# Kernel tuning notes

Hardware: AMD Instinct MI355X
Metric: run time of the kernel (lower is better)

## Reference

```python
import jax, jax.numpy as jnp
import numpy as np

N, D = 32768, 256  # n_nodes, in_dim == mem_dim


def setup_inputs() -> dict:
    key = jax.random.key(0)
    ks = jax.random.split(key, 8)
    inputs = jax.random.normal(ks[0], (N, D), jnp.float32)
    state = jax.random.normal(ks[1], (1, D), jnp.float32)  # initial root cell state
    s = 1.0 / np.sqrt(D)  # pytorch default uniform init bound
    root_W = jax.random.uniform(ks[2], (D, D), jnp.float32, -s, s)
    root_b = jax.random.uniform(ks[3], (D,), jnp.float32, -s, s)
    W_ih = jax.random.uniform(ks[4], (4 * D, D), jnp.float32, -s, s)
    W_hh = jax.random.uniform(ks[5], (4 * D, D), jnp.float32, -s, s)
    b_ih = jax.random.uniform(ks[6], (4 * D,), jnp.float32, -s, s)
    b_hh = jax.random.uniform(ks[7], (4 * D,), jnp.float32, -s, s)
    # topologically ordered random tree: parents[i] < i, node 0 is root
    rng = np.random.default_rng(0)
    raw = rng.integers(0, N, size=N)
    parents = jnp.asarray(np.minimum(raw, np.maximum(np.arange(N) - 1, 0)).astype(np.int64))
    idx = jnp.arange(N, dtype=jnp.int64)  # node -> input row (tree.idx)
    return dict(inputs=inputs, state=state, root_W=root_W, root_b=root_b,
                W_ih=W_ih, W_hh=W_hh, b_ih=b_ih, b_hh=b_hh,
                parents=parents, idx=idx)


def reference(inputs, state, root_W, root_b, W_ih, W_hh, b_ih, b_hh, parents, idx):
    n, d = inputs.shape
    # root: tanh(Linear(inputs[root_idx])), cell state = given state
    h0 = jnp.tanh(inputs[idx[0]] @ root_W.T + root_b)
    c0 = state[0]
    H = jnp.zeros((n, d), inputs.dtype).at[0].set(h0)
    C = jnp.zeros((n, d), inputs.dtype).at[0].set(c0)

    def step(carry, i):
        H, C = carry
        p = parents[i]
        x = inputs[idx[i]]
        # torch nn.LSTMCell: gates = x W_ih^T + b_ih + h W_hh^T + b_hh
        gates = x @ W_ih.T + b_ih + H[p] @ W_hh.T + b_hh
        ig, fg, gg, og = jnp.split(gates, 4)
        c = jax.nn.sigmoid(fg) * C[p] + jax.nn.sigmoid(ig) * jnp.tanh(gg)
        h = jax.nn.sigmoid(og) * jnp.tanh(c)
        return (H.at[i].set(h), C.at[i].set(c)), None

    (H, C), _ = jax.lax.scan(step, (H, C), jnp.arange(1, n))
    # topdown_hidden_traversal: scatter each node's hidden into a [n_inputs, mem_dim] buffer
    hiddens = jnp.zeros((n, d), inputs.dtype).at[idx].set(H)
    # (root topdown_state, root topdown hidden, all hiddens)
    return C[0:1], H[0:1], hiddens
```

## Files before the change

### kernel.cpp

```cpp
#include <hip/hip_runtime.h>


#define NN 32768
#define DD 256
#define GP 1024
#define DSTR 16

typedef __attribute__((ext_vector_type(8))) short short8;
typedef __attribute__((ext_vector_type(4))) float float4_;

static __device__ __forceinline__ unsigned short f2bf(float f) {
    unsigned u = __builtin_bit_cast(unsigned, f);
    unsigned r = u + 0x7FFFu + ((u >> 16) & 1u);
    return (unsigned short)(r >> 16);
}
static __device__ __forceinline__ float bf2f(unsigned short u) {
    unsigned v = ((unsigned)u) << 16;
    return __builtin_bit_cast(float, v);
}
static __device__ __forceinline__ float sigf(float x) { return 1.0f / (1.0f + __expf(-x)); }
static __device__ __forceinline__ float tanh_(float x) { return 1.0f - 2.0f / (__expf(2.0f * x) + 1.0f); }

__global__ void k_init(int* cnt, int* cur, int* done, int* maxd) {
    int g = blockIdx.x * 256 + threadIdx.x;
    if (g < NN + 2) { cnt[g] = 0; cur[g] = 0; }
    if (g < (NN + 2) * DSTR) done[g] = 0;
    if (g == 0) maxd[0] = 0;
}

__global__ void k_root(const float* __restrict__ X, const float* __restrict__ state,
                       const float* __restrict__ rootW, const float* __restrict__ rootb,
                       const int* __restrict__ idx,
                       unsigned short* __restrict__ Hb, float* __restrict__ C, int* __restrict__ done) {
    const int t = threadIdx.x;
    const int row = idx[0];
    const float4_* xr = (const float4_*)(X + (size_t)row * DD);
    const float4_* wr = (const float4_*)(rootW + (size_t)t * DD);
    float acc = rootb[t];
    for (int k = 0; k < DD / 4; ++k) {
        float4_ a = xr[k], b = wr[k];
        acc += a[0] * b[0] + a[1] * b[1] + a[2] * b[2] + a[3] * b[3];
    }
    Hb[t] = f2bf(tanh_(acc));
    C[t] = state[t];
    __syncthreads();
    __threadfence();
    if (t == 0) __hip_atomic_store(&done[0], 8, __ATOMIC_RELEASE, __HIP_MEMORY_SCOPE_AGENT);
}

__global__ void k_dep_init(const int* __restrict__ parents, int* dep, int* jmp) {
    int i = blockIdx.x * 256 + threadIdx.x;
    if (i >= NN) return;
    dep[i] = (i == 0) ? 0 : 1;
    jmp[i] = (i == 0) ? 0 : parents[i];
}

__global__ void k_dep_step(const int* __restrict__ depA, const int* __restrict__ jmpA,
                           int* __restrict__ depB, int* __restrict__ jmpB) {
    int i = blockIdx.x * 256 + threadIdx.x;
    if (i >= NN) return;
    int j = jmpA[i];
    depB[i] = depA[i] + depA[j];
    jmpB[i] = jmpA[j];
}

__global__ void k_hist(const int* __restrict__ dep, int* cnt, int* maxd) {
    int i = blockIdx.x * 256 + threadIdx.x;
    if (i >= NN) return;
    int d = dep[i];
    atomicAdd(&cnt[d], 1);
    atomicMax(&maxd[0], d);
}

__global__ void k_scan(const int* __restrict__ cnt, int* __restrict__ off) {
    __shared__ int sums[256];
    const int tid = threadIdx.x;
    const int base = tid * 128;
    int s = 0;
    for (int k = 0; k < 128; ++k) s += cnt[base + k];
    sums[tid] = s;
    __syncthreads();
    if (tid == 0) {
        int run = 0;
        for (int t = 0; t < 256; ++t) { int tmp = sums[t]; sums[t] = run; run += tmp; }
    }
    __syncthreads();
    int run = sums[tid];
    for (int k = 0; k < 128; ++k) { off[base + k] = run; run += cnt[base + k]; }
    if (tid == 255) off[NN] = run;
}

__global__ void k_scatter(const int* __restrict__ dep, const int* __restrict__ off,
                          int* cur, int* __restrict__ lev) {
    int i = blockIdx.x * 256 + threadIdx.x;
    if (i >= NN) return;
    int d = dep[i];
    int pos = off[d] + atomicAdd(&cur[d], 1);
    lev[pos] = i;
}

__global__ __launch_bounds__(256, 1) void k_gx(
    const float* __restrict__ X, const float* __restrict__ Wih,
    const float* __restrict__ bih, const float* __restrict__ bhh,
    const int* __restrict__ idx, unsigned short* __restrict__ Gp) {
    __shared__ __align__(16) short bw_s[128 * 264];
    __shared__ float bias_s[128];
    const int tid = threadIdx.x;
    const int w = tid >> 6, l = tid & 63;
    const int lanelo = l & 15, quad = l >> 4;

    short8 a[2][8];
    #pragma unroll
    for (int ti = 0; ti < 2; ++ti) {
        int n = (blockIdx.x * 8 + w * 2 + ti) * 16 + lanelo;
        int row = idx[n];
        const float* xp = X + (size_t)row * DD + quad * 8;
        #pragma unroll
        for (int ks = 0; ks < 8; ++ks) {
            float4_ x0 = *(const float4_*)(xp + ks * 32);
            float4_ x1 = *(const float4_*)(xp + ks * 32 + 4);
            short8 s;
            s[0] = f2bf(x0[0]); s[1] = f2bf(x0[1]); s[2] = f2bf(x0[2]); s[3] = f2bf(x0[3]);
            s[4] = f2bf(x1[0]); s[5] = f2bf(x1[1]); s[6] = f2bf(x1[2]); s[7] = f2bf(x1[3]);
            a[ti][ks] = s;
        }
    }
    for (int gc = 0; gc < 8; ++gc) {
        __syncthreads();
        for (int e = tid; e < 128 * 64; e += 256) {
            int r = e >> 6, c4 = (e & 63) * 4;
            float4_ b = *(const float4_*)(Wih + (size_t)(gc * 128 + r) * DD + c4);
            unsigned short* pb = (unsigned short*)&bw_s[r * 264 + c4];
            pb[0] = f2bf(b[0]); pb[1] = f2bf(b[1]); pb[2] = f2bf(b[2]); pb[3] = f2bf(b[3]);
        }
        if (tid < 128) bias_s[tid] = bih[gc * 128 + tid] + bhh[gc * 128 + tid];
        __syncthreads();
        #pragma unroll
        for (int ntl = 0; ntl < 8; ++ntl) {
            float4_ acc0 = (float4_){0.f, 0.f, 0.f, 0.f};
            float4_ acc1 = (float4_){0.f, 0.f, 0.f, 0.f};
            #pragma unroll
            for (int ks = 0; ks < 8; ++ks) {
                short8 bf = *(const short8*)&bw_s[(ntl * 16 + lanelo) * 264 + ks * 32 + quad * 8];
                acc0 = __builtin_amdgcn_mfma_f32_16x16x32_bf16(a[0][ks], bf, acc0, 0, 0, 0);
                acc1 = __builtin_amdgcn_mfma_f32_16x16x32_bf16(a[1][ks], bf, acc1, 0, 0, 0);
            }
            float bia = bias_s[ntl * 16 + lanelo];
            int g = gc * 128 + ntl * 16 + lanelo;
            int nb0 = (blockIdx.x * 8 + w * 2) * 16 + quad * 4;
            #pragma unroll
            for (int r = 0; r < 4; ++r) {
                Gp[(size_t)(nb0 + r) * GP + g] = f2bf(acc0[r] + bia);
                Gp[(size_t)(nb0 + 16 + r) * GP + g] = f2bf(acc1[r] + bia);
            }
        }
    }
}

__global__ __launch_bounds__(256, 1) void k_tree2(
    const float* __restrict__ Whh,
    const int* __restrict__ parents,
    const int* __restrict__ off, const int* __restrict__ lev, const int* __restrict__ maxd_g,
    const unsigned short* __restrict__ Gp,
    unsigned short* __restrict__ Hb, float* __restrict__ C, int* __restrict__ done) {

    __shared__ __align__(16) short w_s[128 * 264];
    __shared__ __align__(16) short A_s[16 * 264];
    __shared__ __align__(16) float G_s[16 * 128];
    __shared__ __align__(16) float R_s[16 * 132];
    __shared__ int nd_s[16], par_s[16];

    const int tid = threadIdx.x;
    const int j = blockIdx.x & 7, grp = blockIdx.x >> 3;
    const int w = tid >> 6, l = tid & 63;
    const int lanelo = l & 15, quad = l >> 4;

    for (int e = tid; e < 128 * 64; e += 256) {
        int r = e >> 6, c4 = (e & 63) * 4;
        int G = ((r >> 5) * 256) + j * 32 + (r & 31);
        float4_ b = *(const float4_*)(Whh + (size_t)G * DD + c4);
        unsigned short* pb = (unsigned short*)&w_s[r * 264 + c4];
        pb[0] = f2bf(b[0]); pb[1] = f2bf(b[1]); pb[2] = f2bf(b[2]); pb[3] = f2bf(b[3]);
    }
    __syncthreads();

    const int maxd = maxd_g[0];
    int prev_lo = off[0], lo = off[1];
    for (int d = 1; d <= maxd; ++d) {
        const int hi = off[d + 1];
        const int tiles = (hi - lo + 15) >> 4;
        if (grp < tiles) {
            const int target = ((lo - prev_lo + 15) >> 4) << 3;
            int ndone = 0;
            for (int t = grp; t < tiles; t += 32) {
                const int base = lo + t * 16;
                if (tid < 16) {
                    int node = -1, p = 0;
                    if (base + tid < hi) { node = lev[base + tid]; p = parents[node]; }
                    nd_s[tid] = node; par_s[tid] = p;
                }
                __syncthreads();
                {
                    int m = tid >> 4, q8 = (tid & 15) * 8;
                    int seg = q8 >> 5, cc = q8 & 31;
                    float4_ g01 = (float4_){0.f, 0.f, 0.f, 0.f};
                    float4_ g23 = (float4_){0.f, 0.f, 0.f, 0.f};
                    if (nd_s[m] >= 0) {
                        const unsigned short* gp =
                            Gp + (size_t)nd_s[m] * GP + seg * 256 + j * 32 + cc;
                        short8 gv = *(const short8*)gp;
                        g01[0] = bf2f(gv[0]); g01[1] = bf2f(gv[1]); g01[2] = bf2f(gv[2]); g01[3] = bf2f(gv[3]);
                        g23[0] = bf2f(gv[4]); g23[1] = bf2f(gv[5]); g23[2] = bf2f(gv[6]); g23[3] = bf2f(gv[7]);
                    }
                    *(float4_*)&G_s[m * 128 + q8] = g01;
                    *(float4_*)&G_s[m * 128 + q8 + 4] = g23;
                }
                if (t == grp) {
                    if (tid == 0) {
                        while (__hip_atomic_load(&done[(d - 1) * DSTR], __ATOMIC_RELAXED,
                                                 __HIP_MEMORY_SCOPE_AGENT) < target)
                            __builtin_amdgcn_s_sleep(1);
                    }
                    __syncthreads();
                    __builtin_amdgcn_fence(__ATOMIC_ACQUIRE, "workgroup");
                }
                float cp0, cp1;
                {
                    int m0 = tid >> 5, c0 = tid & 31, col = j * 32 + c0;
                    cp0 = __hip_atomic_load(&C[(size_t)par_s[m0] * DD + col],
                                            __ATOMIC_RELAXED, __HIP_MEMORY_SCOPE_AGENT);
                    cp1 = __hip_atomic_load(&C[(size_t)par_s[m0 + 8] * DD + col],
                                            __ATOMIC_RELAXED, __HIP_MEMORY_SCOPE_AGENT);
                }
                {
                    const unsigned* HbU = (const unsigned*)Hb;
                    unsigned hv[8];
                    #pragma unroll
                    for (int k2 = 0; k2 < 8; ++k2) {
                        int e = tid + k2 * 256, m = e >> 7, cu = e & 127;
                        hv[k2] = (nd_s[m] >= 0)
                            ? __hip_atomic_load(&HbU[(size_t)par_s[m] * 128 + cu],
                                                __ATOMIC_RELAXED, __HIP_MEMORY_SCOPE_AGENT)
                            : 0u;
                    }
                    #pragma unroll
                    for (int k2 = 0; k2 < 8; ++k2) {
                        int e = tid + k2 * 256, m = e >> 7, cu = e & 127;
                        *(unsigned*)&A_s[m * 264 + cu * 2] = hv[k2];
                    }
                }
                __syncthreads();
                {
                    short8 af[8];
                    #pragma unroll
                    for (int ks = 0; ks < 8; ++ks)
                        af[ks] = *(const short8*)&A_s[lanelo * 264 + ks * 32 + quad * 8];
                    #pragma unroll
                    for (int ti = 0; ti < 2; ++ti) {
                        int ntl = w * 2 + ti;
                        float4_ acc = (float4_){0.f, 0.f, 0.f, 0.f};
                        #pragma unroll
                        for (int ks = 0; ks < 8; ++ks) {
                            short8 bf = *(const short8*)&w_s[(ntl * 16 + lanelo) * 264 + ks * 32 + quad * 8];
                            acc = __builtin_amdgcn_mfma_f32_16x16x32_bf16(af[ks], bf, acc, 0, 0, 0);
                        }
                        #pragma unroll
                        for (int r = 0; r < 4; ++r)
                            R_s[(quad * 4 + r) * 132 + ntl * 16 + lanelo] = acc[r];
                    }
                }
                __syncthreads();
                {
                    int m0 = tid >> 5, c = tid & 31, col = j * 32 + c;
                    #pragma unroll
                    for (int pass = 0; pass < 2; ++pass) {
                        int m = m0 + pass * 8;
                        float cp = pass ? cp1 : cp0;
                        float ig = R_s[m * 132 + c]      + G_s[m * 128 + c];
                        float fg = R_s[m * 132 + 32 + c] + G_s[m * 128 + 32 + c];
                        float gg = R_s[m * 132 + 64 + c] + G_s[m * 128 + 64 + c];
                        float og = R_s[m * 132 + 96 + c] + G_s[m * 128 + 96 + c];
                        float cn = sigf(fg) * cp + sigf(ig) * tanh_(gg);
                        float hn = sigf(og) * tanh_(cn);
                        int node = nd_s[m];
                        unsigned short hs = f2bf(hn);
                        unsigned pair = ((unsigned)hs) |
                                        (((unsigned)(unsigned short)__shfl_down((int)hs, 1)) << 16);
                        if (node >= 0) {
                            __hip_atomic_store(&C[(size_t)node * DD + col], cn,
                                               __ATOMIC_RELAXED, __HIP_MEMORY_SCOPE_AGENT);
                            if ((c & 1) == 0)
                                __hip_atomic_store(&((unsigned*)Hb)[(size_t)node * 128 + (col >> 1)],
                                                   pair, __ATOMIC_RELAXED, __HIP_MEMORY_SCOPE_AGENT);
                        }
                    }
                }
                ndone++;
                __syncthreads();
            }
            __builtin_amdgcn_fence(__ATOMIC_RELEASE, "workgroup");
            if (tid == 0)
                __hip_atomic_fetch_add(&done[d * DSTR], ndone,
                                       __ATOMIC_RELAXED, __HIP_MEMORY_SCOPE_AGENT);
        }
        prev_lo = lo; lo = hi;
    }
}

__global__ void k_out(const unsigned short* __restrict__ Hb, const float* __restrict__ C,
                      const int* __restrict__ idx, float* __restrict__ out) {
    const int b = blockIdx.x, t = threadIdx.x;
    if (b < NN) {
        int drow = idx[b];
        out[512 + (size_t)drow * DD + t] = bf2f(Hb[(size_t)b * DD + t]);
    } else {
        out[t] = C[t];
        out[DD + t] = bf2f(Hb[t]);
    }
}

extern "C" void kernel_launch(void* const* d_in, const int* in_sizes, int n_in,
                              void* d_out, int out_size, void* d_ws, size_t ws_size,
                              hipStream_t stream) {
    const float* X     = (const float*)d_in[0];
    const float* state = (const float*)d_in[1];
    const float* rootW = (const float*)d_in[2];
    const float* rootb = (const float*)d_in[3];
    const float* Wih   = (const float*)d_in[4];
    const float* Whh   = (const float*)d_in[5];
    const float* bih   = (const float*)d_in[6];
    const float* bhh   = (const float*)d_in[7];
    const int* parents = (const int*)d_in[8];
    const int* idx     = (const int*)d_in[9];

    float* C           = (float*)d_ws;
    unsigned short* Hb = (unsigned short*)(C + (size_t)NN * DD);
    unsigned short* Gp = Hb + (size_t)NN * DD;
    int* ip            = (int*)(Gp + (size_t)NN * GP);
    int* depA = ip;            ip += NN;
    int* jmpA = ip;            ip += NN;
    int* depB = ip;            ip += NN;
    int* jmpB = ip;            ip += NN;
    int* cnt  = ip;            ip += NN + 2;
    int* off  = ip;            ip += NN + 2;
    int* cur  = ip;            ip += NN + 2;
    int* lev  = ip;            ip += NN;
    int* done = ip;            ip += (NN + 2) * DSTR;
    int* maxd = ip;            ip += 4;
    float* out = (float*)d_out;

    k_init<<<dim3(((NN + 2) * DSTR + 255) / 256), dim3(256), 0, stream>>>(cnt, cur, done, maxd);
    k_root<<<dim3(1), dim3(256), 0, stream>>>(X, state, rootW, rootb, idx, Hb, C, done);

    k_dep_init<<<dim3(128), dim3(256), 0, stream>>>(parents, depA, jmpA);
    int* dA = depA; int* jA = jmpA; int* dB = depB; int* jB = jmpB;
    for (int it = 0; it < 15; ++it) {
        k_dep_step<<<dim3(128), dim3(256), 0, stream>>>(dA, jA, dB, jB);
        int* tp;
        tp = dA; dA = dB; dB = tp;
        tp = jA; jA = jB; jB = tp;
    }
    k_hist<<<dim3(128), dim3(256), 0, stream>>>(dA, cnt, maxd);
    k_scan<<<dim3(1), dim3(256), 0, stream>>>(cnt, off);
    k_scatter<<<dim3(128), dim3(256), 0, stream>>>(dA, off, cur, lev);

    k_gx<<<dim3(256), dim3(256), 0, stream>>>(X, Wih, bih, bhh, idx, Gp);
    k_tree2<<<dim3(256), dim3(256), 0, stream>>>(Whh, parents, off, lev, maxd, Gp, Hb, C, done);
    k_out<<<dim3(NN + 1), dim3(256), 0, stream>>>(Hb, C, idx, out);
}
```

Measured before the change: 1.760 ms.

## Replace per-level done counters with sentinel-based per-parent dataflow readiness

Removes the per-depth completion counters and the level-wide barrier wait. Instead, C and H are pre-filled with sentinel values, and each tile spins until its parents' rows no longer hold sentinels. A tile can then start as soon as its own parents are ready rather than waiting for the whole previous level. This adds a full-buffer sentinel fill in k_init and a retry loop with block-wide votes. It relies on the computed values never equalling the sentinel bit patterns.

```diff
diff --git a/kernel.cpp b/kernel.cpp
--- a/kernel.cpp
+++ b/kernel.cpp
@@ -4,10 +4,12 @@
 #define NN 32768
 #define DD 256
 #define GP 1024
-#define DSTR 16
+#define SENT_C 0x7FC00001u
+#define SENT_H 0xFFFFFFFFu
 
 typedef __attribute__((ext_vector_type(8))) short short8;
 typedef __attribute__((ext_vector_type(4))) float float4_;
+typedef __attribute__((ext_vector_type(4))) unsigned uint4_;
 
 static __device__ __forceinline__ unsigned short f2bf(float f) {
     unsigned u = __builtin_bit_cast(unsigned, f);
@@ -21,17 +23,24 @@
 static __device__ __forceinline__ float sigf(float x) { return 1.0f / (1.0f + __expf(-x)); }
 static __device__ __forceinline__ float tanh_(float x) { return 1.0f - 2.0f / (__expf(2.0f * x) + 1.0f); }
 
-__global__ void k_init(int* cnt, int* cur, int* done, int* maxd) {
-    int g = blockIdx.x * 256 + threadIdx.x;
+__global__ void k_init(int* cnt, int* cur, int* maxd, float* C, unsigned* HbU) {
+    const int g = blockIdx.x * 256 + threadIdx.x;
     if (g < NN + 2) { cnt[g] = 0; cur[g] = 0; }
-    if (g < (NN + 2) * DSTR) done[g] = 0;
     if (g == 0) maxd[0] = 0;
+    const uint4_ sc = (uint4_){SENT_C, SENT_C, SENT_C, SENT_C};
+    const uint4_ sh = (uint4_){SENT_H, SENT_H, SENT_H, SENT_H};
+    uint4_* Cu = (uint4_*)C;
+    uint4_* Hu = (uint4_*)HbU;
+    #pragma unroll
+    for (int k = 0; k < 4; ++k) Cu[(size_t)g + (size_t)k * 524288] = sc;
+    #pragma unroll
+    for (int k = 0; k < 2; ++k) Hu[(size_t)g + (size_t)k * 524288] = sh;
 }
 
 __global__ void k_root(const float* __restrict__ X, const float* __restrict__ state,
                        const float* __restrict__ rootW, const float* __restrict__ rootb,
                        const int* __restrict__ idx,
-                       unsigned short* __restrict__ Hb, float* __restrict__ C, int* __restrict__ done) {
+                       unsigned short* __restrict__ Hb, float* __restrict__ C) {
     const int t = threadIdx.x;
     const int row = idx[0];
     const float4_* xr = (const float4_*)(X + (size_t)row * DD);
@@ -43,9 +52,6 @@
     }
     Hb[t] = f2bf(tanh_(acc));
     C[t] = state[t];
-    __syncthreads();
-    __threadfence();
-    if (t == 0) __hip_atomic_store(&done[0], 8, __ATOMIC_RELEASE, __HIP_MEMORY_SCOPE_AGENT);
 }
 
 __global__ void k_dep_init(const int* __restrict__ parents, int* dep, int* jmp) {
@@ -162,7 +168,7 @@
     const int* __restrict__ parents,
     const int* __restrict__ off, const int* __restrict__ lev, const int* __restrict__ maxd_g,
     const unsigned short* __restrict__ Gp,
-    unsigned short* __restrict__ Hb, float* __restrict__ C, int* __restrict__ done) {
+    unsigned short* __restrict__ Hb, float* __restrict__ C) {
 
     __shared__ __align__(16) short w_s[128 * 264];
     __shared__ __align__(16) short A_s[16 * 264];
@@ -184,126 +190,123 @@
     }
     __syncthreads();
 
+    const unsigned* HbU = (const unsigned*)Hb;
     const int maxd = maxd_g[0];
-    int prev_lo = off[0], lo = off[1];
+    int lo = off[1];
     for (int d = 1; d <= maxd; ++d) {
         const int hi = off[d + 1];
         const int tiles = (hi - lo + 15) >> 4;
-        if (grp < tiles) {
-            const int target = ((lo - prev_lo + 15) >> 4) << 3;
-            int ndone = 0;
-            for (int t = grp; t < tiles; t += 32) {
-                const int base = lo + t * 16;
-                if (tid < 16) {
-                    int node = -1, p = 0;
-                    if (base + tid < hi) { node = lev[base + tid]; p = parents[node]; }
-                    nd_s[tid] = node; par_s[tid] = p;
+        for (int t = grp; t < tiles; t += 32) {
+            const int base = lo + t * 16;
+            if (tid < 16) {
+                int node = -1, p = 0;
+                if (base + tid < hi) { node = lev[base + tid]; p = parents[node]; }
+                nd_s[tid] = node; par_s[tid] = p;
+            }
+            __syncthreads();
+            {
+                int m = tid >> 4, q8 = (tid & 15) * 8;
+                int seg = q8 >> 5, cc = q8 & 31;
+                float4_ g01 = (float4_){0.f, 0.f, 0.f, 0.f};
+                float4_ g23 = (float4_){0.f, 0.f, 0.f, 0.f};
+                if (nd_s[m] >= 0) {
+                    const unsigned short* gp =
+                        Gp + (size_t)nd_s[m] * GP + seg * 256 + j * 32 + cc;
+                    short8 gv = *(const short8*)gp;
+                    g01[0] = bf2f(gv[0]); g01[1] = bf2f(gv[1]); g01[2] = bf2f(gv[2]); g01[3] = bf2f(gv[3]);
+                    g23[0] = bf2f(gv[4]); g23[1] = bf2f(gv[5]); g23[2] = bf2f(gv[6]); g23[3] = bf2f(gv[7]);
                 }
-                __syncthreads();
-                {
-                    int m = tid >> 4, q8 = (tid & 15) * 8;
-                    int seg = q8 >> 5, cc = q8 & 31;
-                    float4_ g01 = (float4_){0.f, 0.f, 0.f, 0.f};
-                    float4_ g23 = (float4_){0.f, 0.f, 0.f, 0.f};
-                    if (nd_s[m] >= 0) {
-                        const unsigned short* gp =
-                            Gp + (size_t)nd_s[m] * GP + seg * 256 + j * 32 + cc;
-                        short8 gv = *(const short8*)gp;
-                        g01[0] = bf2f(gv[0]); g01[1] = bf2f(gv[1]); g01[2] = bf2f(gv[2]); g01[3] = bf2f(gv[3]);
-                        g23[0] = bf2f(gv[4]); g23[1] = bf2f(gv[5]); g23[2] = bf2f(gv[6]); g23[3] = bf2f(gv[7]);
-                    }
-                    *(float4_*)&G_s[m * 128 + q8] = g01;
-                    *(float4_*)&G_s[m * 128 + q8 + 4] = g23;
-                }
-                if (t == grp) {
-                    if (tid == 0) {
-                        while (__hip_atomic_load(&done[(d - 1) * DSTR], __ATOMIC_RELAXED,
-                                                 __HIP_MEMORY_SCOPE_AGENT) < target)
-                            __builtin_amdgcn_s_sleep(1);
-                    }
-                    __syncthreads();
-                    __builtin_amdgcn_fence(__ATOMIC_ACQUIRE, "workgroup");
-                }
-                float cp0, cp1;
-                {
-                    int m0 = tid >> 5, c0 = tid & 31, col = j * 32 + c0;
+                *(float4_*)&G_s[m * 128 + q8] = g01;
+                *(float4_*)&G_s[m * 128 + q8 + 4] = g23;
+            }
+            if (tid == 0) {
+                const unsigned* sp = &HbU[(size_t)par_s[0] * 128 + j * 16];
+                while (__hip_atomic_load(sp, __ATOMIC_RELAXED, __HIP_MEMORY_SCOPE_AGENT) == SENT_H)
+                    __builtin_amdgcn_s_sleep(1);
+            }
+            __syncthreads();
+            const int m0 = tid >> 5, c0 = tid & 31, col = j * 32 + c0;
+            float cp0 = 0.f, cp1 = 0.f;
+            unsigned hv[8];
+            bool ok = false;
+            while (true) {
+                if (!ok) {
+                    bool good = true;
                     cp0 = __hip_atomic_load(&C[(size_t)par_s[m0] * DD + col],
                                             __ATOMIC_RELAXED, __HIP_MEMORY_SCOPE_AGENT);
                     cp1 = __hip_atomic_load(&C[(size_t)par_s[m0 + 8] * DD + col],
                                             __ATOMIC_RELAXED, __HIP_MEMORY_SCOPE_AGENT);
-                }
-                {
-                    const unsigned* HbU = (const unsigned*)Hb;
-                    unsigned hv[8];
+                    if (nd_s[m0] >= 0 && __builtin_bit_cast(unsigned, cp0) == SENT_C) good = false;
+                    if (nd_s[m0 + 8] >= 0 && __builtin_bit_cast(unsigned, cp1) == SENT_C) good = false;
                     #pragma unroll
                     for (int k2 = 0; k2 < 8; ++k2) {
-                        int e = tid + k2 * 256, m = e >> 7, cu = e & 127;
-                        hv[k2] = (nd_s[m] >= 0)
-                            ? __hip_atomic_load(&HbU[(size_t)par_s[m] * 128 + cu],
-                                                __ATOMIC_RELAXED, __HIP_MEMORY_SCOPE_AGENT)
-                            : 0u;
+                        const int e = tid + k2 * 256, m = e >> 7, cu = e & 127;
+                        if (nd_s[m] >= 0) {
+                            hv[k2] = __hip_atomic_load(&HbU[(size_t)par_s[m] * 128 + cu],
+                                                       __ATOMIC_RELAXED, __HIP_MEMORY_SCOPE_AGENT);
+                            if (hv[k2] == SENT_H) good = false;
+                        } else {
+                            hv[k2] = 0u;
+                        }
+                    }
+                    ok = good;
+                }
+                if (__syncthreads_and(ok ? 1 : 0)) break;
+                __builtin_amdgcn_s_sleep(1);
+            }
+            #pragma unroll
+            for (int k2 = 0; k2 < 8; ++k2) {
+                const int e = tid + k2 * 256, m = e >> 7, cu = e & 127;
+                *(unsigned*)&A_s[m * 264 + cu * 2] = hv[k2];
+            }
+            __syncthreads();
+            {
+                short8 af[8];
+                #pragma unroll
+                for (int ks = 0; ks < 8; ++ks)
+                    af[ks] = *(const short8*)&A_s[lanelo * 264 + ks * 32 + quad * 8];
+                #pragma unroll
+                for (int ti = 0; ti < 2; ++ti) {
+                    int ntl = w * 2 + ti;
+                    float4_ acc = (float4_){0.f, 0.f, 0.f, 0.f};
+                    #pragma unroll
+                    for (int ks = 0; ks < 8; ++ks) {
+                        short8 bf = *(const short8*)&w_s[(ntl * 16 + lanelo) * 264 + ks * 32 + quad * 8];
+                        acc = __builtin_amdgcn_mfma_f32_16x16x32_bf16(af[ks], bf, acc, 0, 0, 0);
                     }
                     #pragma unroll
-                    for (int k2 = 0; k2 < 8; ++k2) {
-                        int e = tid + k2 * 256, m = e >> 7, cu = e & 127;
-                        *(unsigned*)&A_s[m * 264 + cu * 2] = hv[k2];
+                    for (int r = 0; r < 4; ++r)
+                        R_s[(quad * 4 + r) * 132 + ntl * 16 + lanelo] = acc[r];
+                }
+            }
+            __syncthreads();
+            {
+                #pragma unroll
+                for (int pass = 0; pass < 2; ++pass) {
+                    int m = m0 + pass * 8;
+                    float cp = pass ? cp1 : cp0;
+                    float ig = R_s[m * 132 + c0]      + G_s[m * 128 + c0];
+                    float fg = R_s[m * 132 + 32 + c0] + G_s[m * 128 + 32 + c0];
+                    float gg = R_s[m * 132 + 64 + c0] + G_s[m * 128 + 64 + c0];
+                    float og = R_s[m * 132 + 96 + c0] + G_s[m * 128 + 96 + c0];
+                    float cn = sigf(fg) * cp + sigf(ig) * tanh_(gg);
+                    float hn = sigf(og) * tanh_(cn);
+                    int node = nd_s[m];
+                    unsigned short hs = f2bf(hn);
+                    unsigned pair = ((unsigned)hs) |
+                                    (((unsigned)(unsigned short)__shfl_down((int)hs, 1)) << 16);
+                    if (node >= 0) {
+                        __hip_atomic_store(&C[(size_t)node * DD + col], cn,
+                                           __ATOMIC_RELAXED, __HIP_MEMORY_SCOPE_AGENT);
+                        if ((c0 & 1) == 0)
+                            __hip_atomic_store(&((unsigned*)Hb)[(size_t)node * 128 + (col >> 1)],
+                                               pair, __ATOMIC_RELAXED, __HIP_MEMORY_SCOPE_AGENT);
                     }
                 }
-                __syncthreads();
-                {
-                    short8 af[8];
-                    #pragma unroll
-                    for (int ks = 0; ks < 8; ++ks)
-                        af[ks] = *(const short8*)&A_s[lanelo * 264 + ks * 32 + quad * 8];
-                    #pragma unroll
-                    for (int ti = 0; ti < 2; ++ti) {
-                        int ntl = w * 2 + ti;
-                        float4_ acc = (float4_){0.f, 0.f, 0.f, 0.f};
-                        #pragma unroll
-                        for (int ks = 0; ks < 8; ++ks) {
-                            short8 bf = *(const short8*)&w_s[(ntl * 16 + lanelo) * 264 + ks * 32 + quad * 8];
-                            acc = __builtin_amdgcn_mfma_f32_16x16x32_bf16(af[ks], bf, acc, 0, 0, 0);
-                        }
-                        #pragma unroll
-                        for (int r = 0; r < 4; ++r)
-                            R_s[(quad * 4 + r) * 132 + ntl * 16 + lanelo] = acc[r];
-                    }
-                }
-                __syncthreads();
-                {
-                    int m0 = tid >> 5, c = tid & 31, col = j * 32 + c;
-                    #pragma unroll
-                    for (int pass = 0; pass < 2; ++pass) {
-                        int m = m0 + pass * 8;
-                        float cp = pass ? cp1 : cp0;
-                        float ig = R_s[m * 132 + c]      + G_s[m * 128 + c];
-                        float fg = R_s[m * 132 + 32 + c] + G_s[m * 128 + 32 + c];
-                        float gg = R_s[m * 132 + 64 + c] + G_s[m * 128 + 64 + c];
-                        float og = R_s[m * 132 + 96 + c] + G_s[m * 128 + 96 + c];
-                        float cn = sigf(fg) * cp + sigf(ig) * tanh_(gg);
-                        float hn = sigf(og) * tanh_(cn);
-                        int node = nd_s[m];
-                        unsigned short hs = f2bf(hn);
-                        unsigned pair = ((unsigned)hs) |
-                                        (((unsigned)(unsigned short)__shfl_down((int)hs, 1)) << 16);
-                        if (node >= 0) {
-                            __hip_atomic_store(&C[(size_t)node * DD + col], cn,
-                                               __ATOMIC_RELAXED, __HIP_MEMORY_SCOPE_AGENT);
-                            if ((c & 1) == 0)
-                                __hip_atomic_store(&((unsigned*)Hb)[(size_t)node * 128 + (col >> 1)],
-                                                   pair, __ATOMIC_RELAXED, __HIP_MEMORY_SCOPE_AGENT);
-                        }
-                    }
-                }
-                ndone++;
-                __syncthreads();
-            }
-            __builtin_amdgcn_fence(__ATOMIC_RELEASE, "workgroup");
-            if (tid == 0)
-                __hip_atomic_fetch_add(&done[d * DSTR], ndone,
-                                       __ATOMIC_RELAXED, __HIP_MEMORY_SCOPE_AGENT);
+            }
+            __syncthreads();
         }
-        prev_lo = lo; lo = hi;
+        lo = hi;
     }
 }
 
@@ -345,12 +348,11 @@
     int* off  = ip;            ip += NN + 2;
     int* cur  = ip;            ip += NN + 2;
     int* lev  = ip;            ip += NN;
-    int* done = ip;            ip += (NN + 2) * DSTR;
     int* maxd = ip;            ip += 4;
     float* out = (float*)d_out;
 
-    k_init<<<dim3(((NN + 2) * DSTR + 255) / 256), dim3(256), 0, stream>>>(cnt, cur, done, maxd);
-    k_root<<<dim3(1), dim3(256), 0, stream>>>(X, state, rootW, rootb, idx, Hb, C, done);
+    k_init<<<dim3(2048), dim3(256), 0, stream>>>(cnt, cur, maxd, C, (unsigned*)Hb);
+    k_root<<<dim3(1), dim3(256), 0, stream>>>(X, state, rootW, rootb, idx, Hb, C);
 
     k_dep_init<<<dim3(128), dim3(256), 0, stream>>>(parents, depA, jmpA);
     int* dA = depA; int* jA = jmpA; int* dB = depB; int* jB = jmpB;
@@ -365,6 +367,6 @@
     k_scatter<<<dim3(128), dim3(256), 0, stream>>>(dA, off, cur, lev);
 
     k_gx<<<dim3(256), dim3(256), 0, stream>>>(X, Wih, bih, bhh, idx, Gp);
-    k_tree2<<<dim3(256), dim3(256), 0, stream>>>(Whh, parents, off, lev, maxd, Gp, Hb, C, done);
+    k_tree2<<<dim3(256), dim3(256), 0, stream>>>(Whh, parents, off, lev, maxd, Gp, Hb, C);
     k_out<<<dim3(NN + 1), dim3(256), 0, stream>>>(Hb, C, idx, out);
 }
```

Result: slower. 2.540 ms (+44.3%).
